# Optimization experiments

Hardware: AMD Instinct MI355X
Metric: run time of the kernel (lower is better)

The kernel has to match this reference:

```python
import jax, jax.numpy as jnp
import numpy as np


def dht(x):
    # Discrete Hartley transform along last axis: DHT(x) = Re(FFT) - Im(FFT)
    X = jnp.fft.fft(x, axis=-1)
    return (X.real - X.imag).astype(x.dtype)


def idht(x):
    # Inverse DHT = DHT / N
    n = x.shape[-1]
    return dht(x) / n


def setup_inputs() -> dict:
    key = jax.random.key(0)
    k1, k2 = jax.random.split(key)
    B, Cin, Cout, N, M = 16, 64, 64, 16384, 64
    x = jax.random.normal(k1, (B, Cin, N), dtype=jnp.float32)
    scale = 1.0 / (Cin * Cout)
    weights1 = scale * jax.random.uniform(k2, (Cout, Cin, M), dtype=jnp.float32)
    return {"x": x, "weights1": weights1, "modes1": M}


def reference(x, weights1, modes1):
    # x: [B, Cin, N]; weights1: [Cout, Cin, M]
    B, Cin, N = x.shape
    Cout = weights1.shape[0]
    x_ht = dht(x)                                  # [B, Cin, N]
    # Mode-wise channel contraction on the first `modes1` Hartley modes
    low = jnp.einsum('bim,oim->bom', x_ht[:, :, :modes1], weights1)  # [B, Cout, M]
    out_ht = jnp.zeros((B, Cout, N), dtype=x.dtype).at[:, :, :modes1].set(low)
    return idht(out_ht)                            # [B, Cout, N]
```

## Files before the change

kernel.cpp:

```cpp
#include <hip/hip_runtime.h>
#include <math.h>

#define N_FFT 16384
#define HALF 8192
#define ROWS 1024
#define KS_A 64
#define KR_A 128
#define CHUNK 32


__global__ __launch_bounds__(256) void k_tab(float* __restrict__ castab) {
    int i = blockIdx.x * 256 + threadIdx.x;
    if (i < N_FFT) {
        double ang = 6.283185307179586476925287 * (double)i / (double)N_FFT;
        castab[i] = (float)(cos(ang) + sin(ang));
    }
}

__global__ __launch_bounds__(256) void k_fill(const float* __restrict__ castab,
                                              float* __restrict__ casAp,
                                              float* __restrict__ casB) {
    int tid = blockIdx.x * 256 + threadIdx.x;
    if (tid < (1 << 19)) {
        int n = tid >> 6, c = tid & 63;
        int m = (c < 32) ? (2 * c) : (2 * (c - 32) + 1);
        casAp[tid] = castab[(n * m) & (N_FFT - 1)];
    } else {
        int t2 = tid - (1 << 19);
        int m = t2 >> 13, n = t2 & (HALF - 1);
        casB[t2] = castab[(m * n) & (N_FFT - 1)];
    }
}

__global__ __launch_bounds__(512, 4) void kA(const float* __restrict__ x,
                                             const float* __restrict__ casAp,
                                             float* __restrict__ partial) {
    const int rb = blockIdx.x & 7;
    const int ks = blockIdx.x >> 3;
    const int rowbase = rb << 7;
    const int kbase = ks * KR_A;

    __shared__ float xs[CHUNK][2][128];

    const int t   = threadIdx.x;
    const int wq  = __builtin_amdgcn_readfirstlane(t >> 6);
    const int lam = t & 63;
    const int c0  = wq * 8;
    const int p   = wq >> 2;
    const int r2  = lam * 2;

    float acc[2][8];
#pragma unroll
    for (int i = 0; i < 2; ++i)
#pragma unroll
        for (int j = 0; j < 8; ++j) acc[i][j] = 0.f;

    for (int ch = 0; ch < KR_A / CHUNK; ++ch) {
        const int k0 = kbase + ch * CHUNK;
        if (ch) __syncthreads();
#pragma unroll
        for (int it = 0; it < 2; ++it) {
            const int idx = it * 512 + t;
            const int r = idx >> 3, kq = idx & 7;
            const float4 a4 = *reinterpret_cast<const float4*>(
                &x[(size_t)(rowbase + r) * N_FFT + k0 + kq * 4]);
            const float4 b4 = *reinterpret_cast<const float4*>(
                &x[(size_t)(rowbase + r) * N_FFT + k0 + kq * 4 + HALF]);
            const int rsw = r ^ (kq << 1);
#pragma unroll
            for (int u = 0; u < 4; ++u) {
                const float a = reinterpret_cast<const float*>(&a4)[u];
                const float b = reinterpret_cast<const float*>(&b4)[u];
                xs[kq * 4 + u][0][rsw] = a + b;
                xs[kq * 4 + u][1][rsw] = a - b;
            }
        }
        __syncthreads();

        const float* cw = casAp + ((size_t)k0 << 6) + c0;
#pragma unroll 4
        for (int k = 0; k < CHUNK; ++k) {
            const int rd = r2 ^ ((k >> 2) << 1);
            const float2 xv = *reinterpret_cast<const float2*>(&xs[k][p][rd]);
            float cv[8];
#pragma unroll
            for (int j = 0; j < 8; ++j) cv[j] = cw[k * 64 + j];
#pragma unroll
            for (int j = 0; j < 8; ++j) {
                acc[0][j] = fmaf(xv.x, cv[j], acc[0][j]);
                acc[1][j] = fmaf(xv.y, cv[j], acc[1][j]);
            }
        }
    }

#pragma unroll
    for (int i = 0; i < 2; ++i) {
        float* pp = &partial[((size_t)ks << 16) +
                             (size_t)(rowbase + r2 + i) * 64 + c0];
        *reinterpret_cast<float4*>(pp) =
            make_float4(acc[i][0], acc[i][1], acc[i][2], acc[i][3]);
        *reinterpret_cast<float4*>(pp + 4) =
            make_float4(acc[i][4], acc[i][5], acc[i][6], acc[i][7]);
    }
}

__global__ __launch_bounds__(256) void kR(const float* __restrict__ partial,
                                          float* __restrict__ xh) {
    const int idx = blockIdx.x * 256 + threadIdx.x;
    const int r = idx >> 6, c = idx & 63;
    const int m = (c < 32) ? (2 * c) : (2 * (c - 32) + 1);
    float a0 = 0.f, a1 = 0.f, a2 = 0.f, a3 = 0.f;
#pragma unroll 4
    for (int sp = 0; sp < KS_A; sp += 4) {
        a0 += partial[((size_t)(sp + 0) << 16) + idx];
        a1 += partial[((size_t)(sp + 1) << 16) + idx];
        a2 += partial[((size_t)(sp + 2) << 16) + idx];
        a3 += partial[((size_t)(sp + 3) << 16) + idx];
    }
    xh[(r << 6) + m] = (a0 + a1) + (a2 + a3);
}

__global__ __launch_bounds__(256) void kB(const float* __restrict__ xh,
                                          const float* __restrict__ w,
                                          float* __restrict__ lowT) {
    const int b  = blockIdx.x >> 4;
    const int og = blockIdx.x & 15;
    const int o  = og * 4 + (threadIdx.x >> 6);
    const int m  = threadIdx.x & 63;
    float a0 = 0.f, a1 = 0.f, a2 = 0.f, a3 = 0.f;
#pragma unroll 4
    for (int i = 0; i < 64; i += 4) {
        a0 = fmaf(xh[(size_t)((b * 64 + i + 0) << 6) + m], w[(size_t)((o * 64 + i + 0) << 6) + m], a0);
        a1 = fmaf(xh[(size_t)((b * 64 + i + 1) << 6) + m], w[(size_t)((o * 64 + i + 1) << 6) + m], a1);
        a2 = fmaf(xh[(size_t)((b * 64 + i + 2) << 6) + m], w[(size_t)((o * 64 + i + 2) << 6) + m], a2);
        a3 = fmaf(xh[(size_t)((b * 64 + i + 3) << 6) + m], w[(size_t)((o * 64 + i + 3) << 6) + m], a3);
    }
    lowT[(size_t)m * ROWS + b * 64 + o] = ((a0 + a1) + (a2 + a3)) * (1.0f / (float)N_FFT);
}

__global__ __launch_bounds__(256, 4) void kC(const float* __restrict__ lowT,
                                             const float* __restrict__ casB,
                                             float* __restrict__ out) {
    const int rb = blockIdx.x >> 5;
    const int nb = blockIdx.x & 31;
    const int t  = threadIdx.x;
    const int wq = __builtin_amdgcn_readfirstlane(t >> 6);
    const int r0 = rb * 32 + wq * 8;
    const int n  = (nb << 8) + (t & 63) * 4;

    float se[8][4], so[8][4];
#pragma unroll
    for (int j = 0; j < 8; ++j)
#pragma unroll
        for (int q = 0; q < 4; ++q) { se[j][q] = 0.f; so[j][q] = 0.f; }

#pragma unroll 2
    for (int m = 0; m < 64; m += 2) {
        const float* lpe = lowT + ((size_t)m << 10) + r0;
        const float* lpo = lpe + ROWS;
        const float4 ce = *reinterpret_cast<const float4*>(&casB[((size_t)m << 13) + n]);
        const float4 co = *reinterpret_cast<const float4*>(&casB[((size_t)(m + 1) << 13) + n]);
        const float cev[4] = {ce.x, ce.y, ce.z, ce.w};
        const float cov[4] = {co.x, co.y, co.z, co.w};
#pragma unroll
        for (int j = 0; j < 8; ++j) {
            const float le = lpe[j];
            const float lo = lpo[j];
#pragma unroll
            for (int q = 0; q < 4; ++q) {
                se[j][q] = fmaf(le, cev[q], se[j][q]);
                so[j][q] = fmaf(lo, cov[q], so[j][q]);
            }
        }
    }

#pragma unroll
    for (int j = 0; j < 8; ++j) {
        const size_t row = (size_t)r0 + j;
        *reinterpret_cast<float4*>(&out[row * N_FFT + n]) =
            make_float4(se[j][0] + so[j][0], se[j][1] + so[j][1],
                        se[j][2] + so[j][2], se[j][3] + so[j][3]);
        *reinterpret_cast<float4*>(&out[row * N_FFT + HALF + n]) =
            make_float4(se[j][0] - so[j][0], se[j][1] - so[j][1],
                        se[j][2] - so[j][2], se[j][3] - so[j][3]);
    }
}

extern "C" void kernel_launch(void* const* d_in, const int* in_sizes, int n_in,
                              void* d_out, int out_size, void* d_ws, size_t ws_size,
                              hipStream_t stream) {
    const float* x = (const float*)d_in[0];
    const float* w = (const float*)d_in[1];
    float* out = (float*)d_out;
    float* ws  = (float*)d_ws;

    float* castab  = ws;
    float* casAp   = ws + 16384;
    float* casB    = ws + 540672;
    float* partial = ws + 1064960;
    float* xh      = ws + 5259264;
    float* lowT    = ws + 5324800;

    k_tab<<<64, 256, 0, stream>>>(castab);
    k_fill<<<4096, 256, 0, stream>>>(castab, casAp, casB);
    kA<<<512, 512, 0, stream>>>(x, casAp, partial);
    kR<<<256, 256, 0, stream>>>(partial, xh);
    kB<<<256, 256, 0, stream>>>(xh, w, lowT);
    kC<<<1024, 256, 0, stream>>>(lowT, casB, out);
}
```

Baseline: 77.01 us.

## Generate Hartley basis by Chebyshev recurrence instead of precomputed cas tables

Drops the k_fill kernel and the large casAp/casB tables. kA and kC now produce cas(2πkm/N) on the fly with the three-term recurrence c_{k+1} = 2cos(θ)·c_k − c_{k−1}, seeded from a small cas/cos table. This removes the global loads of basis values and one launch, at the cost of extra FMAs and float rounding that builds up along the recurrence. kC is also retiled to 16 rows by 1 column per thread with scalar stores.

```diff
diff --git a/kernel.cpp b/kernel.cpp
--- a/kernel.cpp
+++ b/kernel.cpp
@@ -7,33 +7,21 @@
 #define KS_A 64
 #define KR_A 128
 #define CHUNK 32
-
-
-__global__ __launch_bounds__(256) void k_tab(float* __restrict__ castab) {
+#define NMASK 16383
+
+
+__global__ __launch_bounds__(256) void k_tab(float* __restrict__ castab,
+                                             float* __restrict__ costab) {
     int i = blockIdx.x * 256 + threadIdx.x;
-    if (i < N_FFT) {
-        double ang = 6.283185307179586476925287 * (double)i / (double)N_FFT;
-        castab[i] = (float)(cos(ang) + sin(ang));
-    }
-}
-
-__global__ __launch_bounds__(256) void k_fill(const float* __restrict__ castab,
-                                              float* __restrict__ casAp,
-                                              float* __restrict__ casB) {
-    int tid = blockIdx.x * 256 + threadIdx.x;
-    if (tid < (1 << 19)) {
-        int n = tid >> 6, c = tid & 63;
-        int m = (c < 32) ? (2 * c) : (2 * (c - 32) + 1);
-        casAp[tid] = castab[(n * m) & (N_FFT - 1)];
-    } else {
-        int t2 = tid - (1 << 19);
-        int m = t2 >> 13, n = t2 & (HALF - 1);
-        casB[t2] = castab[(m * n) & (N_FFT - 1)];
-    }
+    double ang = 6.283185307179586476925287 * (double)i / (double)N_FFT;
+    double c = cos(ang), s = sin(ang);
+    castab[i] = (float)(c + s);
+    costab[i] = (float)(2.0 * c);
 }
 
 __global__ __launch_bounds__(512, 4) void kA(const float* __restrict__ x,
-                                             const float* __restrict__ casAp,
+                                             const float* __restrict__ castab,
+                                             const float* __restrict__ costab,
                                              float* __restrict__ partial) {
     const int rb = blockIdx.x & 7;
     const int ks = blockIdx.x >> 3;
@@ -48,12 +36,20 @@
     const int c0  = wq * 8;
     const int p   = wq >> 2;
     const int r2  = lam * 2;
-
-    float acc[2][8];
-#pragma unroll
-    for (int i = 0; i < 2; ++i)
-#pragma unroll
-        for (int j = 0; j < 8; ++j) acc[i][j] = 0.f;
+    const int mbase = (wq < 4) ? (wq << 4) : (((wq - 4) << 4) + 1);
+
+    float k2[8], cA[8], cB[8];
+#pragma unroll
+    for (int j = 0; j < 8; ++j) {
+        const int m = mbase + 2 * j;
+        k2[j] = costab[m];
+        cB[j] = castab[((kbase - 1) * m) & NMASK];
+        cA[j] = castab[(kbase * m) & NMASK];
+    }
+
+    float acc0[8], acc1[8];
+#pragma unroll
+    for (int j = 0; j < 8; ++j) { acc0[j] = 0.f; acc1[j] = 0.f; }
 
     for (int ch = 0; ch < KR_A / CHUNK; ++ch) {
         const int k0 = kbase + ch * CHUNK;
@@ -77,18 +73,26 @@
         }
         __syncthreads();
 
-        const float* cw = casAp + ((size_t)k0 << 6) + c0;
-#pragma unroll 4
-        for (int k = 0; k < CHUNK; ++k) {
-            const int rd = r2 ^ ((k >> 2) << 1);
-            const float2 xv = *reinterpret_cast<const float2*>(&xs[k][p][rd]);
-            float cv[8];
-#pragma unroll
-            for (int j = 0; j < 8; ++j) cv[j] = cw[k * 64 + j];
-#pragma unroll
-            for (int j = 0; j < 8; ++j) {
-                acc[0][j] = fmaf(xv.x, cv[j], acc[0][j]);
-                acc[1][j] = fmaf(xv.y, cv[j], acc[1][j]);
+        for (int k = 0; k < CHUNK; k += 2) {
+            {
+                const int rd = r2 ^ ((k >> 2) << 1);
+                const float2 s2 = *reinterpret_cast<const float2*>(&xs[k][p][rd]);
+#pragma unroll
+                for (int j = 0; j < 8; ++j) {
+                    acc0[j] = fmaf(s2.x, cA[j], acc0[j]);
+                    acc1[j] = fmaf(s2.y, cA[j], acc1[j]);
+                    cB[j] = fmaf(k2[j], cA[j], -cB[j]);
+                }
+            }
+            {
+                const int rd = r2 ^ (((k + 1) >> 2) << 1);
+                const float2 s2 = *reinterpret_cast<const float2*>(&xs[k + 1][p][rd]);
+#pragma unroll
+                for (int j = 0; j < 8; ++j) {
+                    acc0[j] = fmaf(s2.x, cB[j], acc0[j]);
+                    acc1[j] = fmaf(s2.y, cB[j], acc1[j]);
+                    cA[j] = fmaf(k2[j], cB[j], -cA[j]);
+                }
             }
         }
     }
@@ -97,10 +101,11 @@
     for (int i = 0; i < 2; ++i) {
         float* pp = &partial[((size_t)ks << 16) +
                              (size_t)(rowbase + r2 + i) * 64 + c0];
+        const float* a = i ? acc1 : acc0;
         *reinterpret_cast<float4*>(pp) =
-            make_float4(acc[i][0], acc[i][1], acc[i][2], acc[i][3]);
+            make_float4(a[0], a[1], a[2], a[3]);
         *reinterpret_cast<float4*>(pp + 4) =
-            make_float4(acc[i][4], acc[i][5], acc[i][6], acc[i][7]);
+            make_float4(a[4], a[5], a[6], a[7]);
     }
 }
 
@@ -139,50 +144,42 @@
 }
 
 __global__ __launch_bounds__(256, 4) void kC(const float* __restrict__ lowT,
-                                             const float* __restrict__ casB,
+                                             const float* __restrict__ castab,
+                                             const float* __restrict__ costab,
                                              float* __restrict__ out) {
-    const int rb = blockIdx.x >> 5;
-    const int nb = blockIdx.x & 31;
+    const int nb = blockIdx.x & 127;
+    const int rb = blockIdx.x >> 7;
     const int t  = threadIdx.x;
     const int wq = __builtin_amdgcn_readfirstlane(t >> 6);
-    const int r0 = rb * 32 + wq * 8;
-    const int n  = (nb << 8) + (t & 63) * 4;
-
-    float se[8][4], so[8][4];
-#pragma unroll
-    for (int j = 0; j < 8; ++j)
-#pragma unroll
-        for (int q = 0; q < 4; ++q) { se[j][q] = 0.f; so[j][q] = 0.f; }
+    const int r0 = rb * 64 + wq * 16;
+    const int n  = (nb << 6) + (t & 63);
+
+    const float k2 = costab[n];
+    float ce = 1.0f;
+    float co = castab[n];
+
+    float se[16], so[16];
+#pragma unroll
+    for (int j = 0; j < 16; ++j) { se[j] = 0.f; so[j] = 0.f; }
 
 #pragma unroll 2
-    for (int m = 0; m < 64; m += 2) {
-        const float* lpe = lowT + ((size_t)m << 10) + r0;
-        const float* lpo = lpe + ROWS;
-        const float4 ce = *reinterpret_cast<const float4*>(&casB[((size_t)m << 13) + n]);
-        const float4 co = *reinterpret_cast<const float4*>(&casB[((size_t)(m + 1) << 13) + n]);
-        const float cev[4] = {ce.x, ce.y, ce.z, ce.w};
-        const float cov[4] = {co.x, co.y, co.z, co.w};
-#pragma unroll
-        for (int j = 0; j < 8; ++j) {
-            const float le = lpe[j];
-            const float lo = lpo[j];
-#pragma unroll
-            for (int q = 0; q < 4; ++q) {
-                se[j][q] = fmaf(le, cev[q], se[j][q]);
-                so[j][q] = fmaf(lo, cov[q], so[j][q]);
-            }
+    for (int g = 0; g < 32; ++g) {
+        const float* le = lowT + ((size_t)(2 * g) << 10) + r0;
+        const float* lo = le + ROWS;
+#pragma unroll
+        for (int j = 0; j < 16; ++j) {
+            se[j] = fmaf(ce, le[j], se[j]);
+            so[j] = fmaf(co, lo[j], so[j]);
         }
-    }
-
-#pragma unroll
-    for (int j = 0; j < 8; ++j) {
+        ce = fmaf(k2, co, -ce);
+        co = fmaf(k2, ce, -co);
+    }
+
+#pragma unroll
+    for (int j = 0; j < 16; ++j) {
         const size_t row = (size_t)r0 + j;
-        *reinterpret_cast<float4*>(&out[row * N_FFT + n]) =
-            make_float4(se[j][0] + so[j][0], se[j][1] + so[j][1],
-                        se[j][2] + so[j][2], se[j][3] + so[j][3]);
-        *reinterpret_cast<float4*>(&out[row * N_FFT + HALF + n]) =
-            make_float4(se[j][0] - so[j][0], se[j][1] - so[j][1],
-                        se[j][2] - so[j][2], se[j][3] - so[j][3]);
+        out[row * N_FFT + n]        = se[j] + so[j];
+        out[row * N_FFT + HALF + n] = se[j] - so[j];
     }
 }
 
@@ -195,16 +192,14 @@
     float* ws  = (float*)d_ws;
 
     float* castab  = ws;
-    float* casAp   = ws + 16384;
-    float* casB    = ws + 540672;
-    float* partial = ws + 1064960;
-    float* xh      = ws + 5259264;
-    float* lowT    = ws + 5324800;
-
-    k_tab<<<64, 256, 0, stream>>>(castab);
-    k_fill<<<4096, 256, 0, stream>>>(castab, casAp, casB);
-    kA<<<512, 512, 0, stream>>>(x, casAp, partial);
+    float* costab  = ws + 16384;
+    float* partial = ws + 32768;
+    float* xh      = ws + 4227072;
+    float* lowT    = ws + 4292608;
+
+    k_tab<<<64, 256, 0, stream>>>(castab, costab);
+    kA<<<512, 512, 0, stream>>>(x, castab, costab, partial);
     kR<<<256, 256, 0, stream>>>(partial, xh);
     kB<<<256, 256, 0, stream>>>(xh, w, lowT);
-    kC<<<1024, 256, 0, stream>>>(lowT, casB, out);
-}
+    kC<<<2048, 256, 0, stream>>>(lowT, castab, costab, out);
+}
```

Result: faster. 66.86 us (-13.2%).
